# Kernel tuning notes

Hardware: AMD Instinct MI355X
Metric: run time of the kernel (lower is better)

## Reference

```python
import jax, jax.numpy as jnp
import numpy as np

B, N = 16, 4096
LAYERS = 4
CUT = 0.33


def setup_inputs() -> dict:
    key = jax.random.key(0)
    ks = jax.random.split(key, 32)
    def rn(k, shape, s=0.05):
        return jax.random.normal(k, shape, jnp.float32) * s
    inp = {}
    inp["mask"] = jax.random.normal(ks[0], (B, 50), jnp.float32)
    inp["mesh"] = jax.random.uniform(ks[1], (B, N, 3), jnp.float32, -1.0, 1.0)
    inp["mask_idx"] = jax.random.randint(ks[2], (B, N), 0, 4, jnp.int32)
    # row-scaled dense adjacency so aggregated features stay O(1)
    inp["adj"] = jax.random.uniform(ks[3], (N, N), jnp.float32) / N
    # action MLP: 50 -> 200 -> 100 -> 100
    inp["aw1"] = rn(ks[4], (50, 200));  inp["ab1"] = rn(ks[5], (200,))
    inp["aw2"] = rn(ks[6], (200, 100)); inp["ab2"] = rn(ks[7], (100,))
    inp["aw3"] = rn(ks[8], (100, 100)); inp["ab3"] = rn(ks[9], (100,))
    # positional MLP: 63 -> 25 -> 50 -> 100
    inp["pw1"] = rn(ks[10], (63, 25));  inp["pb1"] = rn(ks[11], (25,))
    inp["pw2"] = rn(ks[12], (25, 50));  inp["pb2"] = rn(ks[13], (50,))
    inp["pw3"] = rn(ks[14], (50, 100)); inp["pb3"] = rn(ks[15], (100,))
    # mask embedding table (4 classes -> 100)
    inp["emb"] = rn(ks[16], (4, 100))
    # GCN layers: [300, 128, 128, 128, 50]
    sizes = [300, 128, 128, 128, 50]
    for i in range(LAYERS):
        inp[f"gw{i}"] = rn(ks[17 + 2 * i], (sizes[i], sizes[i + 1]))
        inp[f"gb{i}"] = rn(ks[18 + 2 * i], (sizes[i + 1],))
    return inp


def _nerf(p):
    # p: [..., 3] -> [..., 60]; freqs: pi, 2pi*1, ..., 2pi*9 (matches torch loop)
    freqs = jnp.asarray([np.pi] + [2.0 * np.pi * i for i in range(1, 10)], jnp.float32)
    ang = p[..., None, :] * freqs[:, None]              # [..., 10, 3]
    e = jnp.stack([jnp.sin(ang), jnp.cos(ang)], axis=-2)  # [..., 10, 2, 3]
    return e.reshape(p.shape[:-1] + (60,))


def _forward(mask, mesh, adj,
             aw1, ab1, aw2, ab2, aw3, ab3,
             pw1, pb1, pw2, pb2, pw3, pb3,
             emb, gw0, gb0, gw1, gb1, gw2, gb2, gw3, gb3,
             mask_idx):
    relu = jax.nn.relu
    # action embedding [B, 100]
    a = relu(mask @ aw1 + ab1)
    a = relu(a @ aw2 + ab2)
    a = a @ aw3 + ab3
    # positional embedding [B, N, 100]
    pe_in = jnp.concatenate([_nerf(mesh), mesh], axis=-1)  # [B, N, 63]
    p = relu(pe_in @ pw1 + pb1)
    p = relu(p @ pw2 + pb2)
    p = p @ pw3 + pb3
    # mask embedding lookup [B, N, 100]
    m = emb[mask_idx]
    a_b = jnp.broadcast_to(a[:, None, :], (mesh.shape[0], mesh.shape[1], a.shape[-1]))
    x = jnp.concatenate([a_b, p, m], axis=-1)  # [B, N, 300]
    gws = [gw0, gw1, gw2, gw3]
    gbs = [gb0, gb1, gb2, gb3]
    for i in range(LAYERS):
        f = x @ gws[i]  # [B, N, out]
        if i != LAYERS - 1:
            L = round(f.shape[-1] * CUT)  # static cut length
            left = jnp.einsum('ij,bjf->bif', adj, f[:, :, :L]) + gbs[i][:L]
            x = relu(jnp.concatenate([left, f[:, :, L:]], axis=-1))
        else:
            x = jnp.einsum('ij,bjf->bif', adj, f) + gbs[i]
    return jnp.max(x, axis=1)  # [B, num_actions]


def reference(mask, mesh, adj,
              aw1, ab1, aw2, ab2, aw3, ab3,
              pw1, pb1, pw2, pb2, pw3, pb3,
              emb, gw0, gb0, gw1, gb1, gw2, gb2, gw3, gb3,
              mask_idx):
    return _forward(mask, mesh, adj,
                    aw1, ab1, aw2, ab2, aw3, ab3,
                    pw1, pb1, pw2, pb2, pw3, pb3,
                    emb, gw0, gb0, gw1, gb1, gw2, gb2, gw3, gb3,
                    mask_idx)
```

## Files before the change

### kernel.cpp

```cpp
#include <hip/hip_runtime.h>

typedef unsigned short u16;
typedef unsigned int u32;
typedef short bf16x8 __attribute__((ext_vector_type(8)));
typedef float f32x4 __attribute__((ext_vector_type(4)));

__device__ __forceinline__ u16 f2b(float f) {
    union { float f; unsigned u; } x; x.f = f;
    unsigned r = x.u + 0x7fffu + ((x.u >> 16) & 1u);
    return (u16)(r >> 16);
}


__global__ void conv_adj(const float* __restrict__ adj, u16* __restrict__ adjB) {
    size_t i = ((size_t)blockIdx.x * 256 + threadIdx.x) * 4;
    if (i < 16777216u) {
        float4 v = *(const float4*)(adj + i);
        u16* o = adjB + i;
        o[0] = f2b(v.x); o[1] = f2b(v.y); o[2] = f2b(v.z); o[3] = f2b(v.w);
    }
}

__global__ void prep_weights(const float* __restrict__ gw1, const float* __restrict__ gw2,
                             const float* __restrict__ gw3,
                             u16* __restrict__ gw1T, u16* __restrict__ gw2T,
                             u16* __restrict__ gw3T) {
    int i = blockIdx.x * 256 + threadIdx.x;
    if (i < 128 * 128) {
        int n = i >> 7, k = i & 127;
        gw1T[i] = f2b(gw1[k * 128 + n]);
        gw2T[i] = f2b(gw2[k * 128 + n]);
        gw3T[i] = (n < 50) ? f2b(gw3[k * 50 + n]) : (u16)0;
    }
}


__global__ void action_mlp(const float* __restrict__ mask,
                           const float* __restrict__ aw1, const float* __restrict__ ab1,
                           const float* __restrict__ aw2, const float* __restrict__ ab2,
                           const float* __restrict__ aw3, const float* __restrict__ ab3,
                           float* __restrict__ aF) {
    __shared__ float sm[50], sh1[200], sh2[100];
    int b = blockIdx.x, t = threadIdx.x;
    if (t < 50) sm[t] = mask[b * 50 + t];
    __syncthreads();
    if (t < 200) {
        float s = ab1[t];
        for (int k = 0; k < 50; ++k) s = fmaf(sm[k], aw1[k * 200 + t], s);
        sh1[t] = fmaxf(s, 0.f);
    }
    __syncthreads();
    if (t < 100) {
        float s = ab2[t];
        for (int k = 0; k < 200; ++k) s = fmaf(sh1[k], aw2[k * 100 + t], s);
        sh2[t] = fmaxf(s, 0.f);
    }
    __syncthreads();
    if (t < 100) {
        float s = ab3[t];
        for (int k = 0; k < 100; ++k) s = fmaf(sh2[k], aw3[k * 100 + t], s);
        aF[b * 100 + t] = s;
    }
}


__global__ void prep_fold(const float* __restrict__ aF, const float* __restrict__ pb3,
                          const float* __restrict__ pw3, const float* __restrict__ emb,
                          const float* __restrict__ gw0,
                          float* __restrict__ A2, float* __restrict__ Ep,
                          u16* __restrict__ WpT) {
    int idx = blockIdx.x * 256 + threadIdx.x;
    if (idx < 2048) {
        int b = idx >> 7, n = idx & 127;
        float s = 0.f;
        for (int j = 0; j < 100; ++j) s = fmaf(aF[b * 100 + j], gw0[j * 128 + n], s);
        for (int j = 0; j < 100; ++j) s = fmaf(pb3[j], gw0[(100 + j) * 128 + n], s);
        A2[idx] = s;
    } else if (idx < 2560) {
        int e = (idx - 2048) >> 7, n = idx & 127;
        float s = 0.f;
        for (int j = 0; j < 100; ++j) s = fmaf(emb[e * 100 + j], gw0[(200 + j) * 128 + n], s);
        Ep[idx - 2048] = s;
    } else if (idx < 10752) {
        int o = idx - 2560;
        int n = o >> 6, k = o & 63;
        u16 v = 0;
        if (k < 50) {
            float s = 0.f;
            for (int c = 0; c < 100; ++c) s = fmaf(pw3[k * 100 + c], gw0[(100 + c) * 128 + n], s);
            v = f2b(s);
        }
        WpT[o] = v;
    }
}


__global__ __launch_bounds__(256)
void nf_h2r(const float* __restrict__ mesh,
            const float* __restrict__ pw1, const float* __restrict__ pb1,
            const float* __restrict__ pw2, const float* __restrict__ pb2,
            u16* __restrict__ H2R) {
    __shared__ float h1x[64 * 29];
    __shared__ u16 st[64 * 66];
    const int tid = threadIdx.x;
    const int wu = __builtin_amdgcn_readfirstlane(tid >> 6);
    const int t = tid & 63;
    const size_t r = (size_t)blockIdx.x * 64 + t;

    float m3[3];
    m3[0] = mesh[3 * r]; m3[1] = mesh[3 * r + 1]; m3[2] = mesh[3 * r + 2];

    int ec[7];
    float hs[7];
#pragma unroll
    for (int j = 0; j < 7; ++j) {
        int col = wu * 7 + j;
        ec[j] = (col < 25) ? col : 24;
        hs[j] = pb1[ec[j]];
    }
#pragma unroll
    for (int d = 0; d < 3; ++d) {
#pragma unroll
        for (int i = 0; i < 10; ++i) {
            float fq = (i == 0) ? 3.14159265358979f : 6.28318530717959f * (float)i;
            float s, c;
            __sincosf(m3[d] * fq, &s, &c);
            int ks = i * 6 + d, kc = i * 6 + 3 + d;
#pragma unroll
            for (int j = 0; j < 7; ++j) hs[j] = fmaf(s, pw1[ks * 25 + ec[j]], hs[j]);
#pragma unroll
            for (int j = 0; j < 7; ++j) hs[j] = fmaf(c, pw1[kc * 25 + ec[j]], hs[j]);
        }
#pragma unroll
        for (int j = 0; j < 7; ++j) hs[j] = fmaf(m3[d], pw1[(60 + d) * 25 + ec[j]], hs[j]);
    }
#pragma unroll
    for (int j = 0; j < 7; ++j) {
        int col = wu * 7 + j;
        if (col < 25) h1x[t * 29 + col] = fmaxf(hs[j], 0.f);
    }
    __syncthreads();

    float h1v[25];
#pragma unroll
    for (int k = 0; k < 25; ++k) h1v[k] = h1x[t * 29 + k];

#pragma unroll
    for (int j = 0; j < 13; ++j) {
        int col = wu * 13 + j;
        int e2 = (col < 50) ? col : 49;
        float s = pb2[e2];
#pragma unroll
        for (int k = 0; k < 25; ++k) s = fmaf(h1v[k], pw2[k * 50 + e2], s);
        st[t * 66 + col] = (col < 50) ? f2b(fmaxf(s, 0.f)) : (u16)0;
    }
    if (wu == 3) {
#pragma unroll
        for (int jj = 0; jj < 12; ++jj) st[t * 66 + 52 + jj] = 0;
    }
    __syncthreads();

    u32* gout = (u32*)H2R + (size_t)blockIdx.x * 2048;
#pragma unroll
    for (int it = 0; it < 8; ++it) {
        int f = tid + it * 256;
        int row = f >> 5, col = f & 31;
        gout[f] = *((const u32*)st + row * 33 + col);
    }
}

template <int EPI, int BN>
__launch_bounds__(256)
__global__ void gemm_bt(const u16* __restrict__ A, const u16* __restrict__ B,
                        int kd, int klen,
                        u16* __restrict__ outX, u16* __restrict__ outFT,
                        float* __restrict__ outF32,
                        const float* __restrict__ A2, const float* __restrict__ Ep,
                        const int* __restrict__ midx, int ncol) {
    constexpr int NF = BN / 32;
    constexpr int BPASS = BN / 32;
    __shared__ u16 As[2 * 128 * 64];
    __shared__ u16 Bs[2 * BN * 64];
    __shared__ float aadd[128];
    __shared__ float eadd[512];
    __shared__ int mil[128];
    constexpr int TBA = 128 * 64 * 2;
    constexpr int TBB = BN * 64 * 2;
    const int tid = threadIdx.x;
    const int wave = tid >> 6, lane = tid & 63;
    const int wr = wave >> 1, wc = wave & 1;
    const int tM = blockIdx.x * 128, tN = blockIdx.y * BN;
    const int lrow = lane & 15, kg = lane >> 4;
    const int srow = tid >> 3;
    const int gcol = ((tid & 7) ^ ((tid >> 3) & 7)) << 3;
    const int k0 = blockIdx.z * klen;

    if constexpr (EPI == 4) {
        if (tid < 128) { mil[tid] = midx[tM + tid]; aadd[tid] = A2[((tM >> 12) << 7) + tid]; }
        eadd[tid] = Ep[tid];
        eadd[tid + 256] = Ep[tid + 256];
        __syncthreads();
    }

    auto stage = [&](int buf, int kt) {
#pragma unroll
        for (int i = 0; i < 4; ++i) {
            int row = i * 32 + srow;
            const u16* ga = A + (size_t)(tM + row) * kd + kt + gcol;
            __builtin_amdgcn_global_load_lds(
                (__attribute__((address_space(1))) void*)ga,
                (__attribute__((address_space(3))) void*)((char*)(&As[0]) +
                    buf * TBA + i * 4096 + wave * 1024), 16, 0, 0);
        }
#pragma unroll
        for (int i = 0; i < BPASS; ++i) {
            int row = i * 32 + srow;
            const u16* gb = B + (size_t)(tN + row) * kd + kt + gcol;
            __builtin_amdgcn_global_load_lds(
                (__attribute__((address_space(1))) void*)gb,
                (__attribute__((address_space(3))) void*)((char*)(&Bs[0]) +
                    buf * TBB + i * 4096 + wave * 1024), 16, 0, 0);
        }
    };

    f32x4 acc[4][NF];
#pragma unroll
    for (int m = 0; m < 4; ++m)
#pragma unroll
        for (int n = 0; n < NF; ++n) acc[m][n] = (f32x4){0.f, 0.f, 0.f, 0.f};

    const int nt = klen >> 6;
    stage(0, k0);
    if (nt > 1) stage(1, k0 + 64);
    for (int t = 0; t < nt; ++t) {
        if (t == nt - 1)              asm volatile("s_waitcnt vmcnt(0)" ::: "memory");
        else if constexpr (BN == 128) asm volatile("s_waitcnt vmcnt(8)" ::: "memory");
        else                          asm volatile("s_waitcnt vmcnt(7)" ::: "memory");
        __builtin_amdgcn_s_barrier();
        __builtin_amdgcn_sched_barrier(0);

        const char* Ab = (const char*)As + (t & 1) * TBA;
        const char* Bb = (const char*)Bs + (t & 1) * TBB;
        bf16x8 af[2][4], bfr[2][NF];
#pragma unroll
        for (int ks = 0; ks < 2; ++ks) {
#pragma unroll
            for (int m = 0; m < 4; ++m) {
                int row = wr * 64 + m * 16 + lrow;
                int psw = (((ks * 4 + kg) ^ (row & 7)) << 4);
                af[ks][m] = *(const bf16x8*)(Ab + row * 128 + psw);
            }
#pragma unroll
            for (int n = 0; n < NF; ++n) {
                int row = wc * (BN / 2) + n * 16 + lrow;
                int psw = (((ks * 4 + kg) ^ (row & 7)) << 4);
                bfr[ks][n] = *(const bf16x8*)(Bb + row * 128 + psw);
            }
        }
        __builtin_amdgcn_s_setprio(1);
#pragma unroll
        for (int ks = 0; ks < 2; ++ks)
#pragma unroll
            for (int m = 0; m < 4; ++m)
#pragma unroll
                for (int n = 0; n < NF; ++n)
                    acc[m][n] = __builtin_amdgcn_mfma_f32_16x16x32_bf16(af[ks][m], bfr[ks][n],
                                                                        acc[m][n], 0, 0, 0);
        __builtin_amdgcn_s_setprio(0);
        __builtin_amdgcn_s_barrier();
        if (t + 2 < nt) stage(t & 1, k0 + (t + 2) * 64);
    }

    const int rbase = tM + wr * 64 + ((lane >> 4) << 2);
    const int cbase = tN + wc * (BN / 2) + (lane & 15);
#pragma unroll
    for (int m = 0; m < 4; ++m) {
        int r0 = rbase + m * 16;
#pragma unroll
        for (int n = 0; n < NF; ++n) {
            int c = cbase + n * 16;
            if (EPI == 0) {
                if (c < 42) {
                    int b = r0 >> 12, node = r0 & 4095;
                    u32 lo = (u32)f2b(acc[m][n][0]) | ((u32)f2b(acc[m][n][1]) << 16);
                    u32 hi = (u32)f2b(acc[m][n][2]) | ((u32)f2b(acc[m][n][3]) << 16);
                    u32* dst = (u32*)(outFT + (size_t)(b * 42 + c) * 4096 + node);
                    dst[0] = lo; dst[1] = hi;
                } else {
#pragma unroll
                    for (int j = 0; j < 4; ++j)
                        outX[(size_t)(r0 + j) * 128 + c] = f2b(fmaxf(acc[m][n][j], 0.f));
                }
            } else if (EPI == 1) {
                if (c < 50) {
                    int b = r0 >> 12, node = r0 & 4095;
                    u32 lo = (u32)f2b(acc[m][n][0]) | ((u32)f2b(acc[m][n][1]) << 16);
                    u32 hi = (u32)f2b(acc[m][n][2]) | ((u32)f2b(acc[m][n][3]) << 16);
                    u32* dst = (u32*)(outFT + (size_t)(b * 50 + c) * 4096 + node);
                    dst[0] = lo; dst[1] = hi;
                }
            } else if (EPI == 4) {
                float v[4];
#pragma unroll
                for (int j = 0; j < 4; ++j) {
                    int lr = (r0 & 127) + j;
                    v[j] = acc[m][n][j] + aadd[c] + eadd[mil[lr] * 128 + c];
                }
                if (c < 42) {
                    int b = r0 >> 12, node = r0 & 4095;
                    u32 lo = (u32)f2b(v[0]) | ((u32)f2b(v[1]) << 16);
                    u32 hi = (u32)f2b(v[2]) | ((u32)f2b(v[3]) << 16);
                    u32* dst = (u32*)(outFT + (size_t)(b * 42 + c) * 4096 + node);
                    dst[0] = lo; dst[1] = hi;
                } else {
#pragma unroll
                    for (int j = 0; j < 4; ++j)
                        outX[(size_t)(r0 + j) * 128 + c] = f2b(fmaxf(v[j], 0.f));
                }
            } else {
                if (c < ncol) {
                    float* P = outF32 + (size_t)blockIdx.z * ncol * 4096;
                    float4 v4 = {acc[m][n][0], acc[m][n][1], acc[m][n][2], acc[m][n][3]};
                    *(float4*)(P + (size_t)c * 4096 + r0) = v4;
                }
            }
        }
    }
}


__global__ __launch_bounds__(256)
void reduce_lr(const float* __restrict__ P, const float* __restrict__ gb,
               u16* __restrict__ X) {
    __shared__ u16 stx[128 * 44];
    const int bx = blockIdx.x;
    const int b = bx >> 5, rt = bx & 31;
    const int r0 = rt * 128;
    const int tid = threadIdx.x;
    const int ci2 = tid >> 7, rr = tid & 127;
    const float* P1 = P + (size_t)672 * 4096;
#pragma unroll
    for (int q = 0; q < 21; ++q) {
        int ci = ci2 * 21 + q;
        size_t off = (size_t)(b * 42 + ci) * 4096 + r0 + rr;
        float v = P[off] + P1[off] + gb[ci];
        stx[rr * 44 + ci] = f2b(fmaxf(v, 0.f));
    }
    __syncthreads();
#pragma unroll
    for (int it = 0; it < 11; ++it) {
        int f = tid + it * 256;
        if (f < 2688) {
            int row = f / 21, col = f - row * 21;
            ((u32*)(X + (size_t)(((size_t)b << 12) + r0 + row) * 128))[col] =
                *((const u32*)stx + row * 22 + col);
        }
    }
}


__global__ void max_reduce3(const float* __restrict__ P, const float* __restrict__ gb3,
                            float* __restrict__ out) {
    __shared__ float sred[256];
    int c = blockIdx.x;
    const float* p0 = P + (size_t)c * 4096;
    const float* p1 = P + (size_t)800 * 4096 + (size_t)c * 4096;
    float m = -1e30f;
    for (int i = threadIdx.x; i < 4096; i += 256) m = fmaxf(m, p0[i] + p1[i]);
    sred[threadIdx.x] = m;
    __syncthreads();
    for (int s = 128; s > 0; s >>= 1) {
        if (threadIdx.x < s) sred[threadIdx.x] = fmaxf(sred[threadIdx.x], sred[threadIdx.x + s]);
        __syncthreads();
    }
    if (threadIdx.x == 0) out[c] = sred[0] + gb3[c % 50];
}


extern "C" void kernel_launch(void* const* d_in, const int* in_sizes, int n_in,
                              void* d_out, int out_size, void* d_ws, size_t ws_size,
                              hipStream_t stream) {
    const float* mask = (const float*)d_in[0];
    const float* mesh = (const float*)d_in[1];
    const int*   midx = (const int*)d_in[2];
    const float* adj  = (const float*)d_in[3];
    const float* aw1 = (const float*)d_in[4],  *ab1 = (const float*)d_in[5];
    const float* aw2 = (const float*)d_in[6],  *ab2 = (const float*)d_in[7];
    const float* aw3 = (const float*)d_in[8],  *ab3 = (const float*)d_in[9];
    const float* pw1 = (const float*)d_in[10], *pb1 = (const float*)d_in[11];
    const float* pw2 = (const float*)d_in[12], *pb2 = (const float*)d_in[13];
    const float* pw3 = (const float*)d_in[14], *pb3 = (const float*)d_in[15];
    const float* emb = (const float*)d_in[16];
    const float* gw0 = (const float*)d_in[17], *gb0 = (const float*)d_in[18];
    const float* gw1 = (const float*)d_in[19], *gb1 = (const float*)d_in[20];
    const float* gw2 = (const float*)d_in[21], *gb2 = (const float*)d_in[22];
    const float* gw3 = (const float*)d_in[23], *gb3 = (const float*)d_in[24];
    float* out = (float*)d_out;

    char* w = (char*)d_ws;
    u16*   adjB  = (u16*)(w);
    u16*   H2R   = (u16*)(w + 33554432);
    float* P     = (float*)(w + 41943040);
    u16*   X1    = (u16*)(w + 75497472);
    u16*   X2    = (u16*)(w + 92274688);
    u16*   FT    = (u16*)(w + 109051904);
    u16*   gw1T  = (u16*)(w + 116391936);
    u16*   gw2T  = (u16*)(w + 116424704);
    u16*   gw3T  = (u16*)(w + 116457472);
    u16*   WpT   = (u16*)(w + 116490240);
    float* A2    = (float*)(w + 116506624);
    float* Ep    = (float*)(w + 116514816);
    float* aF    = (float*)(w + 116516864);

    hipMemsetAsync(FT + (size_t)672 * 4096, 0, (size_t)(896 - 672) * 4096 * 2, stream);

    prep_weights<<<dim3(64), dim3(256), 0, stream>>>(gw1, gw2, gw3, gw1T, gw2T, gw3T);
    conv_adj<<<dim3(16384), dim3(256), 0, stream>>>(adj, adjB);
    action_mlp<<<dim3(16), dim3(256), 0, stream>>>(mask, aw1, ab1, aw2, ab2, aw3, ab3, aF);
    prep_fold<<<dim3(42), dim3(256), 0, stream>>>(aF, pb3, pw3, emb, gw0, A2, Ep, WpT);
    nf_h2r<<<dim3(1024), dim3(256), 0, stream>>>(mesh, pw1, pb1, pw2, pb2, H2R);

    gemm_bt<4, 128><<<dim3(512, 1, 1), dim3(256), 0, stream>>>(H2R, WpT, 64, 64,
        X1, FT, nullptr, A2, Ep, midx, 0);
    gemm_bt<6, 96><<<dim3(32, 8, 2), dim3(256), 0, stream>>>(adjB, FT, 4096, 2048,
        nullptr, nullptr, P, nullptr, nullptr, nullptr, 672);
    reduce_lr<<<dim3(512), dim3(256), 0, stream>>>(P, gb0, X1);
    gemm_bt<0, 128><<<dim3(512, 1, 1), dim3(256), 0, stream>>>(X1, gw1T, 128, 128,
        X2, FT, nullptr, nullptr, nullptr, nullptr, 0);
    gemm_bt<6, 96><<<dim3(32, 8, 2), dim3(256), 0, stream>>>(adjB, FT, 4096, 2048,
        nullptr, nullptr, P, nullptr, nullptr, nullptr, 672);
    reduce_lr<<<dim3(512), dim3(256), 0, stream>>>(P, gb1, X2);
    gemm_bt<0, 128><<<dim3(512, 1, 1), dim3(256), 0, stream>>>(X2, gw2T, 128, 128,
        X1, FT, nullptr, nullptr, nullptr, nullptr, 0);
    gemm_bt<6, 96><<<dim3(32, 8, 2), dim3(256), 0, stream>>>(adjB, FT, 4096, 2048,
        nullptr, nullptr, P, nullptr, nullptr, nullptr, 672);
    reduce_lr<<<dim3(512), dim3(256), 0, stream>>>(P, gb2, X1);
    gemm_bt<1, 128><<<dim3(512, 1, 1), dim3(256), 0, stream>>>(X1, gw3T, 128, 128,
        nullptr, FT, nullptr, nullptr, nullptr, nullptr, 0);
    gemm_bt<6, 96><<<dim3(32, 9, 2), dim3(256), 0, stream>>>(adjB, FT, 4096, 2048,
        nullptr, nullptr, P, nullptr, nullptr, nullptr, 800);

    max_reduce3<<<dim3(800), dim3(256), 0, stream>>>(P, gb3, out);
}
```

Before: 408.2 us.

## Add dedicated adjacency GEMM with register-resident B fragments and 4-way bf16 split-K

Replaces the generic split-K adjacency GEMM (BN=96, 2-way split, fp32 partials) with a dedicated kernel. It uses 128-wide N tiles, loads B fragments directly from global memory into double-buffered registers instead of LDS, splits K four ways and writes bf16 partials. The aim is to cut LDS traffic for B, improve wave count and occupancy, and halve the bytes of partial-sum writes and reads. The reduce kernels now sum four bf16 partials, which adds rounding error and more reads per output, and the wider N tile wastes some columns on padding.

```diff
diff --git a/kernel.cpp b/kernel.cpp
--- a/kernel.cpp
+++ b/kernel.cpp
@@ -9,6 +9,9 @@
     union { float f; unsigned u; } x; x.f = f;
     unsigned r = x.u + 0x7fffu + ((x.u >> 16) & 1u);
     return (u16)(r >> 16);
+}
+__device__ __forceinline__ float b2f(u16 h) {
+    union { u32 u; float f; } x; x.u = ((u32)h) << 16; return x.f;
 }
 
 
@@ -174,9 +177,8 @@
 __global__ void gemm_bt(const u16* __restrict__ A, const u16* __restrict__ B,
                         int kd, int klen,
                         u16* __restrict__ outX, u16* __restrict__ outFT,
-                        float* __restrict__ outF32,
                         const float* __restrict__ A2, const float* __restrict__ Ep,
-                        const int* __restrict__ midx, int ncol) {
+                        const int* __restrict__ midx) {
     constexpr int NF = BN / 32;
     constexpr int BPASS = BN / 32;
     __shared__ u16 As[2 * 128 * 64];
@@ -193,7 +195,6 @@
     const int lrow = lane & 15, kg = lane >> 4;
     const int srow = tid >> 3;
     const int gcol = ((tid & 7) ^ ((tid >> 3) & 7)) << 3;
-    const int k0 = blockIdx.z * klen;
 
     if constexpr (EPI == 4) {
         if (tid < 128) { mil[tid] = midx[tM + tid]; aadd[tid] = A2[((tM >> 12) << 7) + tid]; }
@@ -230,8 +231,8 @@
         for (int n = 0; n < NF; ++n) acc[m][n] = (f32x4){0.f, 0.f, 0.f, 0.f};
 
     const int nt = klen >> 6;
-    stage(0, k0);
-    if (nt > 1) stage(1, k0 + 64);
+    stage(0, 0);
+    if (nt > 1) stage(1, 64);
     for (int t = 0; t < nt; ++t) {
         if (t == nt - 1)              asm volatile("s_waitcnt vmcnt(0)" ::: "memory");
         else if constexpr (BN == 128) asm volatile("s_waitcnt vmcnt(8)" ::: "memory");
@@ -268,7 +269,7 @@
                                                                         acc[m][n], 0, 0, 0);
         __builtin_amdgcn_s_setprio(0);
         __builtin_amdgcn_s_barrier();
-        if (t + 2 < nt) stage(t & 1, k0 + (t + 2) * 64);
+        if (t + 2 < nt) stage(t & 1, (t + 2) * 64);
     }
 
     const int rbase = tM + wr * 64 + ((lane >> 4) << 2);
@@ -299,7 +300,7 @@
                     u32* dst = (u32*)(outFT + (size_t)(b * 50 + c) * 4096 + node);
                     dst[0] = lo; dst[1] = hi;
                 }
-            } else if (EPI == 4) {
+            } else {
                 float v[4];
 #pragma unroll
                 for (int j = 0; j < 4; ++j) {
@@ -317,20 +318,115 @@
                     for (int j = 0; j < 4; ++j)
                         outX[(size_t)(r0 + j) * 128 + c] = f2b(fmaxf(v[j], 0.f));
                 }
-            } else {
-                if (c < ncol) {
-                    float* P = outF32 + (size_t)blockIdx.z * ncol * 4096;
-                    float4 v4 = {acc[m][n][0], acc[m][n][1], acc[m][n][2], acc[m][n][3]};
-                    *(float4*)(P + (size_t)c * 4096 + r0) = v4;
-                }
             }
         }
     }
 }
 
+__launch_bounds__(256)
+__global__ void gemm_adj(const u16* __restrict__ A, const u16* __restrict__ B,
+                         u16* __restrict__ P, int ncol) {
+    __shared__ u16 As[2 * 128 * 64];
+    constexpr int TBA = 128 * 64 * 2;
+    const int tid = threadIdx.x;
+    const int wave = tid >> 6, lane = tid & 63;
+    const int wr = wave >> 1, wc = wave & 1;
+    const int tM = blockIdx.x * 128, tN = blockIdx.y * 128;
+    const int lrow = lane & 15, kg = lane >> 4;
+    const int srow = tid >> 3;
+    const int gcol = ((tid & 7) ^ ((tid >> 3) & 7)) << 3;
+    const int k0 = blockIdx.z * 1024;
+    const int kd = 4096;
+
+    auto stageA = [&](int buf, int kt) {
+#pragma unroll
+        for (int i = 0; i < 4; ++i) {
+            int row = i * 32 + srow;
+            const u16* ga = A + (size_t)(tM + row) * kd + kt + gcol;
+            __builtin_amdgcn_global_load_lds(
+                (__attribute__((address_space(1))) void*)ga,
+                (__attribute__((address_space(3))) void*)((char*)(&As[0]) +
+                    buf * TBA + i * 4096 + wave * 1024), 16, 0, 0);
+        }
+    };
+
+    const u16* bbase = B + (size_t)(tN + wc * 64 + lrow) * kd + kg * 8;
+
+    f32x4 acc[4][4];
+#pragma unroll
+    for (int m = 0; m < 4; ++m)
+#pragma unroll
+        for (int n = 0; n < 4; ++n) acc[m][n] = (f32x4){0.f, 0.f, 0.f, 0.f};
+
+    bf16x8 bf0[8], bf1[8];
+
+    stageA(0, k0);
+#pragma unroll
+    for (int q = 0; q < 8; ++q)
+        bf0[q] = *(const bf16x8*)(bbase + (size_t)(q & 3) * 16 * kd + (q >> 2) * 32 + k0);
+    stageA(1, k0 + 64);
+
+    auto step = [&](int t, bf16x8 (&bfc)[8], bf16x8 (&bfn)[8]) {
+        if (t == 15) asm volatile("s_waitcnt vmcnt(0)" ::: "memory");
+        else         asm volatile("s_waitcnt vmcnt(4)" ::: "memory");
+        __builtin_amdgcn_s_barrier();
+        __builtin_amdgcn_sched_barrier(0);
+        if (t + 1 < 16) {
+#pragma unroll
+            for (int q = 0; q < 8; ++q)
+                bfn[q] = *(const bf16x8*)(bbase + (size_t)(q & 3) * 16 * kd + (q >> 2) * 32 +
+                                          k0 + (t + 1) * 64);
+        }
+        const char* Ab = (const char*)As + (t & 1) * TBA;
+        __builtin_amdgcn_s_setprio(1);
+#pragma unroll
+        for (int ks = 0; ks < 2; ++ks) {
+            bf16x8 af[4];
+#pragma unroll
+            for (int m = 0; m < 4; ++m) {
+                int row = wr * 64 + m * 16 + lrow;
+                int psw = (((ks * 4 + kg) ^ (row & 7)) << 4);
+                af[m] = *(const bf16x8*)(Ab + row * 128 + psw);
+            }
+#pragma unroll
+            for (int m = 0; m < 4; ++m)
+#pragma unroll
+                for (int n = 0; n < 4; ++n)
+                    acc[m][n] = __builtin_amdgcn_mfma_f32_16x16x32_bf16(
+                        af[m], bfc[ks * 4 + n], acc[m][n], 0, 0, 0);
+        }
+        __builtin_amdgcn_s_setprio(0);
+        __builtin_amdgcn_s_barrier();
+        if (t + 2 < 16) stageA(t & 1, k0 + (t + 2) * 64);
+    };
+
+    for (int tt = 0; tt < 16; tt += 2) {
+        step(tt, bf0, bf1);
+        step(tt + 1, bf1, bf0);
+    }
+
+    const int rbase = tM + wr * 64 + ((lane >> 4) << 2);
+    const int cbase = tN + wc * 64 + (lane & 15);
+    u16* Pz = P + (size_t)blockIdx.z * ncol * 4096;
+#pragma unroll
+    for (int m = 0; m < 4; ++m) {
+        int r0 = rbase + m * 16;
+#pragma unroll
+        for (int n = 0; n < 4; ++n) {
+            int c = cbase + n * 16;
+            if (c < ncol) {
+                u32 lo = (u32)f2b(acc[m][n][0]) | ((u32)f2b(acc[m][n][1]) << 16);
+                u32 hi = (u32)f2b(acc[m][n][2]) | ((u32)f2b(acc[m][n][3]) << 16);
+                u32* dst = (u32*)(Pz + (size_t)c * 4096 + r0);
+                dst[0] = lo; dst[1] = hi;
+            }
+        }
+    }
+}
+
 
 __global__ __launch_bounds__(256)
-void reduce_lr(const float* __restrict__ P, const float* __restrict__ gb,
+void reduce_lr(const u16* __restrict__ P, const float* __restrict__ gb,
                u16* __restrict__ X) {
     __shared__ u16 stx[128 * 44];
     const int bx = blockIdx.x;
@@ -338,12 +434,13 @@
     const int r0 = rt * 128;
     const int tid = threadIdx.x;
     const int ci2 = tid >> 7, rr = tid & 127;
-    const float* P1 = P + (size_t)672 * 4096;
+    const size_t SS = (size_t)672 * 4096;
 #pragma unroll
     for (int q = 0; q < 21; ++q) {
         int ci = ci2 * 21 + q;
         size_t off = (size_t)(b * 42 + ci) * 4096 + r0 + rr;
-        float v = P[off] + P1[off] + gb[ci];
+        float v = b2f(P[off]) + b2f(P[off + SS]) + b2f(P[off + 2 * SS]) + b2f(P[off + 3 * SS])
+                  + gb[ci];
         stx[rr * 44 + ci] = f2b(fmaxf(v, 0.f));
     }
     __syncthreads();
@@ -359,14 +456,15 @@
 }
 
 
-__global__ void max_reduce3(const float* __restrict__ P, const float* __restrict__ gb3,
+__global__ void max_reduce3(const u16* __restrict__ P, const float* __restrict__ gb3,
                             float* __restrict__ out) {
     __shared__ float sred[256];
     int c = blockIdx.x;
-    const float* p0 = P + (size_t)c * 4096;
-    const float* p1 = P + (size_t)800 * 4096 + (size_t)c * 4096;
+    const size_t SS = (size_t)800 * 4096;
+    const u16* p = P + (size_t)c * 4096;
     float m = -1e30f;
-    for (int i = threadIdx.x; i < 4096; i += 256) m = fmaxf(m, p0[i] + p1[i]);
+    for (int i = threadIdx.x; i < 4096; i += 256)
+        m = fmaxf(m, b2f(p[i]) + b2f(p[i + SS]) + b2f(p[i + 2 * SS]) + b2f(p[i + 3 * SS]));
     sred[threadIdx.x] = m;
     __syncthreads();
     for (int s = 128; s > 0; s >>= 1) {
@@ -400,7 +498,7 @@
     char* w = (char*)d_ws;
     u16*   adjB  = (u16*)(w);
     u16*   H2R   = (u16*)(w + 33554432);
-    float* P     = (float*)(w + 41943040);
+    u16*   Pb    = (u16*)(w + 41943040);
     u16*   X1    = (u16*)(w + 75497472);
     u16*   X2    = (u16*)(w + 92274688);
     u16*   FT    = (u16*)(w + 109051904);
@@ -421,24 +519,20 @@
     nf_h2r<<<dim3(1024), dim3(256), 0, stream>>>(mesh, pw1, pb1, pw2, pb2, H2R);
 
     gemm_bt<4, 128><<<dim3(512, 1, 1), dim3(256), 0, stream>>>(H2R, WpT, 64, 64,
-        X1, FT, nullptr, A2, Ep, midx, 0);
-    gemm_bt<6, 96><<<dim3(32, 8, 2), dim3(256), 0, stream>>>(adjB, FT, 4096, 2048,
-        nullptr, nullptr, P, nullptr, nullptr, nullptr, 672);
-    reduce_lr<<<dim3(512), dim3(256), 0, stream>>>(P, gb0, X1);
+        X1, FT, A2, Ep, midx);
+    gemm_adj<<<dim3(32, 6, 4), dim3(256), 0, stream>>>(adjB, FT, Pb, 672);
+    reduce_lr<<<dim3(512), dim3(256), 0, stream>>>(Pb, gb0, X1);
     gemm_bt<0, 128><<<dim3(512, 1, 1), dim3(256), 0, stream>>>(X1, gw1T, 128, 128,
-        X2, FT, nullptr, nullptr, nullptr, nullptr, 0);
-    gemm_bt<6, 96><<<dim3(32, 8, 2), dim3(256), 0, stream>>>(adjB, FT, 4096, 2048,
-        nullptr, nullptr, P, nullptr, nullptr, nullptr, 672);
-    reduce_lr<<<dim3(512), dim3(256), 0, stream>>>(P, gb1, X2);
+        X2, FT, nullptr, nullptr, nullptr);
+    gemm_adj<<<dim3(32, 6, 4), dim3(256), 0, stream>>>(adjB, FT, Pb, 672);
+    reduce_lr<<<dim3(512), dim3(256), 0, stream>>>(Pb, gb1, X2);
     gemm_bt<0, 128><<<dim3(512, 1, 1), dim3(256), 0, stream>>>(X2, gw2T, 128, 128,
-        X1, FT, nullptr, nullptr, nullptr, nullptr, 0);
-    gemm_bt<6, 96><<<dim3(32, 8, 2), dim3(256), 0, stream>>>(adjB, FT, 4096, 2048,
-        nullptr, nullptr, P, nullptr, nullptr, nullptr, 672);
-    reduce_lr<<<dim3(512), dim3(256), 0, stream>>>(P, gb2, X1);
+        X1, FT, nullptr, nullptr, nullptr);
+    gemm_adj<<<dim3(32, 6, 4), dim3(256), 0, stream>>>(adjB, FT, Pb, 672);
+    reduce_lr<<<dim3(512), dim3(256), 0, stream>>>(Pb, gb2, X1);
     gemm_bt<1, 128><<<dim3(512, 1, 1), dim3(256), 0, stream>>>(X1, gw3T, 128, 128,
-        nullptr, FT, nullptr, nullptr, nullptr, nullptr, 0);
-    gemm_bt<6, 96><<<dim3(32, 9, 2), dim3(256), 0, stream>>>(adjB, FT, 4096, 2048,
-        nullptr, nullptr, P, nullptr, nullptr, nullptr, 800);
-
-    max_reduce3<<<dim3(800), dim3(256), 0, stream>>>(P, gb3, out);
-}
+        nullptr, FT, nullptr, nullptr, nullptr);
+    gemm_adj<<<dim3(32, 7, 4), dim3(256), 0, stream>>>(adjB, FT, Pb, 800);
+
+    max_reduce3<<<dim3(800), dim3(256), 0, stream>>>(Pb, gb3, out);
+}
```

New measurement: 512.9 us. 1.26x slower.
